# Optimization experiments

Measured on AMD Instinct MI355X. Metric: run time of the kernel, lower is better.

Reference implementation:

```python
import jax, jax.numpy as jnp
import numpy as np

B, N, D = 64, 1024, 512
H, LD = 8, 64            # num_heads, linear_hidden_dim (H*LD == D)
HIDDEN = 4 * D           # ffn_multiply = 4.0
NB = 128                 # number of timestamp buckets
EPS = 1e-6
TS_SCALE = NB / 14.0     # log1p(1e6) ~ 13.8 -> buckets span [0, NB]


def rms_norm(x, eps=EPS):
    return x * jax.lax.rsqrt(jnp.mean(x * x, axis=-1, keepdims=True) + eps)


def setup_inputs() -> dict:
    key = jax.random.key(0)
    ks = jax.random.split(key, 8)
    lengths = np.linspace(256, N, B).astype(np.int64)
    x_offsets = jnp.asarray(np.concatenate([[0], np.cumsum(lengths)]), dtype=jnp.int64)
    T = int(lengths.sum())
    x = jax.random.normal(ks[0], (T, D), dtype=jnp.float32)
    all_timestamps = jnp.sort(jax.random.randint(ks[1], (B, N), 0, 10**6, dtype=jnp.int64), axis=1)
    invalid_attn_mask = jnp.tril(jnp.ones((N, N), jnp.float32))  # causal
    uv = jax.random.normal(ks[2], (D, 3 * H * LD), dtype=jnp.float32) * 0.02
    pos_w = jax.random.normal(ks[3], (2 * N - 1,), dtype=jnp.float32) * 0.02
    ts_w = jax.random.normal(ks[4], (NB + 1,), dtype=jnp.float32) * 0.02
    w_ams = jax.random.normal(ks[5], (2 * H * LD, D), dtype=jnp.float32) * 0.02
    w1 = jax.random.normal(ks[6], (D, HIDDEN), dtype=jnp.float32) * 0.02
    w2 = jax.random.normal(ks[7], (HIDDEN, D), dtype=jnp.float32) * 0.02
    return {"x": x, "x_offsets": x_offsets, "all_timestamps": all_timestamps,
            "invalid_attn_mask": invalid_attn_mask, "uv": uv, "pos_w": pos_w,
            "ts_w": ts_w, "w_ams": w_ams, "w1": w1, "w2": w2}


def reference(x, x_offsets, all_timestamps, invalid_attn_mask, uv, pos_w, ts_w, w_ams, w1, w2):
    T = x.shape[0]
    # RMSNorm (no learned scale, matches F.rms_norm with no weight) + fused proj + SiLU
    proj = jax.nn.silu(rms_norm(x) @ uv)                       # [T, 3*H*LD]
    u, v = proj[:, :2 * H * LD], proj[:, 2 * H * LD:]          # [T,2HD'], [T,HD']
    # jagged -> padded dense
    tok = jnp.arange(T)
    seg = jnp.searchsorted(x_offsets, tok, side="right") - 1   # batch id per token
    pos = tok - x_offsets[seg]                                  # position within sequence
    padded_v = jnp.zeros((B, N, H * LD), v.dtype).at[seg, pos].set(v).reshape(B, N, H, LD)
    # positional relative bias (batch-independent)
    rel = jnp.arange(N)[:, None] - jnp.arange(N)[None, :]
    pos_attn = pos_w[rel + N - 1] * invalid_attn_mask           # [N,N]
    # temporal relative bias: log-bucketized |t_i - t_j|
    dt = jnp.abs(all_timestamps[:, :, None] - all_timestamps[:, None, :]).astype(jnp.float32)
    bucket = jnp.clip(jnp.floor(jnp.log1p(dt) * TS_SCALE), 0, NB).astype(jnp.int32)
    ts_attn = ts_w[bucket] * invalid_attn_mask[None]            # [B,N,N]
    # two-stream bias 'attention' (no softmax)
    out_pos = jnp.einsum("nm,bmhd->bnhd", pos_attn, padded_v)
    out_ts = jnp.einsum("bnm,bmhd->bnhd", ts_attn, padded_v)
    combined = jnp.concatenate([out_pos, out_ts], axis=-1).reshape(B, N, 2 * H * LD)
    attn_out = combined[seg, pos]                               # dense -> jagged, [T, 2*H*LD]
    # gated norm + multistage FFN with residuals
    ams = u * rms_norm(attn_out)
    h = x + ams @ w_ams
    out = h + jax.nn.silu(rms_norm(h) @ w1) @ w2
    return out
```

## Files before the change

kernel.cpp:

```cpp
#include <hip/hip_runtime.h>
#include <cmath>


using u16 = unsigned short;

typedef __bf16 bf16x8 __attribute__((ext_vector_type(8)));
typedef float  f32x4  __attribute__((ext_vector_type(4)));

#define TS_SCALE_F (float)(128.0 / 14.0)

__device__ __forceinline__ u16 f2b(float f) {
  unsigned u = __float_as_uint(f);
  unsigned r = 0x7FFFu + ((u >> 16) & 1u);
  return (u16)((u + r) >> 16);
}
__device__ __forceinline__ float b2f(u16 v) {
  return __uint_as_float(((unsigned)v) << 16);
}
__device__ __forceinline__ bf16x8 as_frag(uint4 r) {
  union { uint4 u; bf16x8 v; } c; c.u = r; return c.v;
}

__device__ __forceinline__ void gload_lds16(const u16* g, u16* l) {
  __builtin_amdgcn_global_load_lds(
      (const __attribute__((address_space(1))) unsigned int*)g,
      (__attribute__((address_space(3))) unsigned int*)l, 16, 0, 0);
}

__device__ __forceinline__ size_t ts_base_elems(int b, int nt) {
  return (size_t)b * 589824 + (size_t)(nt * (nt + 1) / 2) * 16384;
}

__global__ __launch_bounds__(256) void wprep(
    const float* __restrict__ W, u16* __restrict__ Wp, int K, int N)
{
  const int p = blockIdx.x, s = blockIdx.y;
  const int t = threadIdx.x;
  size_t base = ((size_t)p * (K >> 5) + s) * 4096;
  const int e0 = t * 16;
  u16 o[16];
#pragma unroll
  for (int i = 0; i < 16; ++i) {
    int e = e0 + i;
    int kb = e >> 10, r = e & 1023, c = r >> 3, ke = r & 7;
    o[i] = f2b(W[(size_t)(s * 32 + kb * 8 + ke) * N + p * 128 + c]);
  }
  *(uint4*)(Wp + base + e0)     = *(uint4*)o;
  *(uint4*)(Wp + base + e0 + 8) = *(uint4*)(o + 8);
}

#define EPI_SILU_BF16 0
#define EPI_ADD_F32   1

template <int EPI>
__global__ __launch_bounds__(256, 2) void gemm_bf16(
    const u16* __restrict__ A, const u16* __restrict__ Wp,
    void* __restrict__ C, const float* __restrict__ ADD,
    int M, int N, int K)
{
  __shared__ u16 lA[128 * 40];
  __shared__ u16 lB[4096];

  const int tid  = threadIdx.x;
  const int c0b  = blockIdx.x;
  const int t0   = blockIdx.y * 128;
  const int c0   = c0b * 128;
  const int wave = tid >> 6, lane = tid & 63;
  const int wr   = (wave >> 1) * 64, wc = (wave & 1) * 64;
  const int l15  = lane & 15, l4 = lane >> 4;

  f32x4 z = {0.f, 0.f, 0.f, 0.f};
  f32x4 acc[4][4];
#pragma unroll
  for (int m = 0; m < 4; ++m)
#pragma unroll
    for (int j = 0; j < 4; ++j) acc[m][j] = z;

  const int ar = tid >> 1, ak = (tid & 1) * 16;
  const bool arow_ok = (t0 + ar) < M;
  const u16* aptr = A + (size_t)(t0 + ar) * K + ak;
  const int ksteps = K >> 5;
  const u16* wpanel = Wp + (size_t)c0b * ksteps * 4096;
  const u16* wsrc = wpanel + wave * 1024 + lane * 8;
  u16* ldsb = &lB[wave * 1024];

  for (int s = 0; s < ksteps; ++s) {
    uint4 a0 = make_uint4(0, 0, 0, 0), a1 = a0;
    if (arow_ok) {
      a0 = *(const uint4*)(aptr);
      a1 = *(const uint4*)(aptr + 8);
    }
    aptr += 32;
    gload_lds16(wsrc, ldsb);
    gload_lds16(wsrc + 512, ldsb + 512);
    wsrc += 4096;
    *(uint4*)&lA[ar * 40 + ak]     = a0;
    *(uint4*)&lA[ar * 40 + ak + 8] = a1;
    __syncthreads();

    bf16x8 af[4], bfv[4];
#pragma unroll
    for (int m = 0; m < 4; ++m)
      af[m] = as_frag(*(const uint4*)&lA[(wr + m * 16 + l15) * 40 + l4 * 8]);
#pragma unroll
    for (int j = 0; j < 4; ++j)
      bfv[j] = as_frag(*(const uint4*)&lB[(l4 << 10) + (wc + j * 16 + l15) * 8]);
#pragma unroll
    for (int m = 0; m < 4; ++m)
#pragma unroll
      for (int j = 0; j < 4; ++j)
        acc[m][j] = __builtin_amdgcn_mfma_f32_16x16x32_bf16(af[m], bfv[j], acc[m][j], 0, 0, 0);
    __syncthreads();
  }

#pragma unroll
  for (int m = 0; m < 4; ++m) {
#pragma unroll
    for (int r = 0; r < 4; ++r) {
      int row = t0 + wr + m * 16 + l4 * 4 + r;
      if (row >= M) continue;
#pragma unroll
      for (int j = 0; j < 4; ++j) {
        int col = c0 + wc + j * 16 + l15;
        size_t idx = (size_t)row * N + col;
        float y = acc[m][j][r];
        if constexpr (EPI == EPI_SILU_BF16) {
          float s = y / (1.f + __expf(-y));
          ((u16*)C)[idx] = f2b(s);
        } else {
          ((float*)C)[idx] = y + ADD[idx];
        }
      }
    }
  }
}

__global__ __launch_bounds__(128) void pos_scores(
    const float* __restrict__ pos_w, u16* __restrict__ pos_s)
{
  const int n = blockIdx.x;
  const int m0 = threadIdx.x * 8;
  u16 o[8];
#pragma unroll
  for (int i = 0; i < 8; ++i) {
    int m = m0 + i;
    float v = (m <= n) ? pos_w[n - m + 1023] : 0.f;
    o[i] = f2b(v);
  }
  *(uint4*)(pos_s + (size_t)n * 1024 + m0) = *(uint4*)o;
}

__global__ __launch_bounds__(256) void ts_scores(
    const int* __restrict__ tstamp, const float* __restrict__ ts_w,
    u16* __restrict__ ts_s)
{
  const int nt = 7 - (blockIdx.x >> 6);
  const int b  = blockIdx.x & 63;
  const int W  = 128 * (nt + 1);
  const int n0 = nt * 128;
  const int tid = threadIdx.x;

  __shared__ float tsw[132];
  __shared__ int   tsm[1024];
  if (tid < 129) tsw[tid] = ts_w[tid];
  for (int i = tid; i < W; i += 256) tsm[i] = tstamp[b * 1024 + i];
  __syncthreads();

  const int r = tid >> 1, h = tid & 1;
  const int n_abs = n0 + r;
  const int t_n = tstamp[b * 1024 + n_abs];
  u16* row = ts_s + ts_base_elems(b, nt) + (size_t)r * W + h * (W >> 1);
  const int c0 = h * (W >> 1);
  const int half = W >> 1;

  for (int c = 0; c < half; c += 8) {
    u16 o[8];
#pragma unroll
    for (int i = 0; i < 8; ++i) {
      int m = c0 + c + i;
      int d = t_n - tsm[m];
      if (d < 0) d = -d;
      float dt = (float)d;
      int bkt = (int)(log1pf(dt) * TS_SCALE_F);
      bkt = bkt > 128 ? 128 : bkt;
      float v = (m <= n_abs) ? tsw[bkt] : 0.f;
      o[i] = f2b(v);
    }
    *(uint4*)(row + c) = *(uint4*)o;
  }
}

__global__ __launch_bounds__(256, 1) void attn_gemm(
    const u16* __restrict__ proj,
    const int* __restrict__ xoff,
    const u16* __restrict__ pos_s,
    const u16* __restrict__ ts_s,
    u16* __restrict__ attn_out,
    int Ttot)
{
  const int flat = blockIdx.x;
  const int nt = 7 - (flat >> 8);
  const int rem = flat & 255;
  const int b  = rem >> 2;
  const int ct = rem & 3;

  const int off = xoff[b];
  int len = xoff[b + 1] - off;
  if (len < 0) len = 0;
  if (len > 1024) len = 1024;
  if (off < 0 || off + len > Ttot) return;
  const int n0 = nt * 128;
  if (n0 >= len) return;
  const int c0 = ct * 128;
  const int W = 128 * (nt + 1);

  __shared__ u16 lP[128 * 40];
  __shared__ u16 lT[128 * 40];
  __shared__ u16 sV[4096];

  const int tid = threadIdx.x;
  const int wave = tid >> 6, lane = tid & 63;
  const int wr = (wave >> 1) * 64, wc = (wave & 1) * 64;
  const int l15 = lane & 15, l4 = lane >> 4;

  f32x4 z = {0.f, 0.f, 0.f, 0.f};
  f32x4 accP[4][4], accT[4][4];
#pragma unroll
  for (int m = 0; m < 4; ++m)
#pragma unroll
    for (int j = 0; j < 4; ++j) { accP[m][j] = z; accT[m][j] = z; }

  const int ar = tid >> 1, ak = (tid & 1) * 16;
  const u16* pRow = pos_s + (size_t)(n0 + ar) * 1024 + ak;
  const u16* tRow = ts_s + ts_base_elems(b, nt) + (size_t)ar * W + ak;
  const int vk = tid >> 3, vc = (tid & 7) * 16;

  const int mEnd = (n0 + 128 < len) ? (n0 + 128) : len;

  for (int m0 = 0; m0 < mEnd; m0 += 32) {
    {
      int mm = m0 + vk;
      uint4 v0 = make_uint4(0, 0, 0, 0), v1 = v0;
      if (mm < len) {
        const u16* src = proj + (size_t)(off + mm) * 1536 + 1024 + c0 + vc;
        v0 = *(const uint4*)src;
        v1 = *(const uint4*)(src + 8);
      }
      u16 tmp[16];
      *(uint4*)tmp       = v0;
      *(uint4*)(tmp + 8) = v1;
      const int kb = vk >> 3, ke = vk & 7;
#pragma unroll
      for (int i = 0; i < 16; ++i) {
        int col = vc + i;
        int o2 = (kb * 2048 + col * 16 + ke * 2) ^ (((col >> 3) & 7) << 4);
        *(u16*)((char*)sV + o2) = tmp[i];
      }
    }
    {
      uint4 p0 = *(const uint4*)(pRow + m0);
      uint4 p1 = *(const uint4*)(pRow + m0 + 8);
      uint4 t0v = *(const uint4*)(tRow + m0);
      uint4 t1v = *(const uint4*)(tRow + m0 + 8);
      int wb = ar * 40 + ak;
      *(uint4*)&lP[wb]     = p0;
      *(uint4*)&lP[wb + 8] = p1;
      *(uint4*)&lT[wb]     = t0v;
      *(uint4*)&lT[wb + 8] = t1v;
    }
    __syncthreads();

    bf16x8 ap[4], at[4], bv[4];
#pragma unroll
    for (int m = 0; m < 4; ++m) {
      ap[m] = as_frag(*(const uint4*)&lP[(wr + m * 16 + l15) * 40 + l4 * 8]);
      at[m] = as_frag(*(const uint4*)&lT[(wr + m * 16 + l15) * 40 + l4 * 8]);
    }
#pragma unroll
    for (int j = 0; j < 4; ++j) {
      int col = wc + j * 16 + l15;
      int o2 = (l4 * 2048 + col * 16) ^ (((col >> 3) & 7) << 4);
      bv[j] = as_frag(*(const uint4*)((char*)sV + o2));
    }
#pragma unroll
    for (int m = 0; m < 4; ++m)
#pragma unroll
      for (int j = 0; j < 4; ++j) {
        accP[m][j] = __builtin_amdgcn_mfma_f32_16x16x32_bf16(ap[m], bv[j], accP[m][j], 0, 0, 0);
        accT[m][j] = __builtin_amdgcn_mfma_f32_16x16x32_bf16(at[m], bv[j], accT[m][j], 0, 0, 0);
      }
    __syncthreads();
  }

#pragma unroll
  for (int m = 0; m < 4; ++m)
#pragma unroll
    for (int r = 0; r < 4; ++r) {
      int n = n0 + wr + m * 16 + l4 * 4 + r;
      if (n >= len) continue;
      size_t t = (size_t)(off + n);
#pragma unroll
      for (int j = 0; j < 4; ++j) {
        int hd = c0 + wc + j * 16 + l15;
        int colP = ((hd >> 6) << 7) + (hd & 63);
        attn_out[t * 1024 + colP]      = f2b(accP[m][j][r]);
        attn_out[t * 1024 + colP + 64] = f2b(accT[m][j][r]);
      }
    }
}

template <int D, bool HASMUL, bool INBF>
__global__ __launch_bounds__(256) void rms_prep(
    const void* __restrict__ in_, const u16* __restrict__ mul, int mulStride,
    u16* __restrict__ out)
{
  const int row = blockIdx.x;
  const int tid = threadIdx.x;
  const float* rf = (const float*)in_ + (INBF ? 0 : (size_t)row * D);
  const u16*   rb = (const u16*)in_ + (INBF ? (size_t)row * D : 0);
  float ss = 0.f;
#pragma unroll
  for (int i = tid; i < D; i += 256) {
    float v = INBF ? b2f(rb[i]) : rf[i];
    ss += v * v;
  }
#pragma unroll
  for (int o = 32; o > 0; o >>= 1) ss += __shfl_down(ss, o, 64);
  __shared__ float sred[4];
  const int wave = tid >> 6, lane = tid & 63;
  if (lane == 0) sred[wave] = ss;
  __syncthreads();
  float inv = rsqrtf((sred[0] + sred[1] + sred[2] + sred[3]) / (float)D + 1e-6f);
#pragma unroll
  for (int i = tid; i < D; i += 256) {
    float v = (INBF ? b2f(rb[i]) : rf[i]) * inv;
    if constexpr (HASMUL) v *= b2f(mul[(size_t)row * mulStride + i]);
    out[(size_t)row * D + i] = f2b(v);
  }
}

extern "C" void kernel_launch(void* const* d_in, const int* in_sizes, int n_in,
                              void* d_out, int out_size, void* d_ws, size_t ws_size,
                              hipStream_t stream)
{
  const float* x      = (const float*)d_in[0];
  const int*   xoff   = (const int*)d_in[1];
  const int*   tstamp = (const int*)d_in[2];
  const float* uv     = (const float*)d_in[4];
  const float* pos_w  = (const float*)d_in[5];
  const float* ts_w   = (const float*)d_in[6];
  const float* w_ams  = (const float*)d_in[7];
  const float* w1     = (const float*)d_in[8];
  const float* w2     = (const float*)d_in[9];
  const int T = in_sizes[0] / 512;

  char* ws = (char*)d_ws;
  size_t o = 0;
  auto take = [&](size_t bytes) { size_t r = o; o += (bytes + 255) & ~(size_t)255; return r; };

  u16* uvb    = (u16*)(ws + take((size_t)512 * 1536 * 2));
  u16* wamsb  = (u16*)(ws + take((size_t)1024 * 512 * 2));
  u16* w1b    = (u16*)(ws + take((size_t)512 * 2048 * 2));
  u16* w2b    = (u16*)(ws + take((size_t)2048 * 512 * 2));
  u16* posS   = (u16*)(ws + take((size_t)1024 * 1024 * 2));

  size_t tsBytes = (size_t)64 * 589824 * 2;
  size_t s2Bytes = (size_t)T * 1024 * 2;
  if (s2Bytes < tsBytes) s2Bytes = tsBytes;
  size_t o_s2 = take(s2Bytes);
  u16* A1   = (u16*)(ws + o_s2);
  u16* tsS  = (u16*)(ws + o_s2);
  u16* A2   = (u16*)(ws + o_s2);
  u16* mid  = (u16*)(ws + o_s2);

  size_t o_proj = take((size_t)T * 1536 * 2);
  u16* proj = (u16*)(ws + o_proj);
  u16* A1p  = proj + (size_t)T * 1024;

  u16*   attnS = (u16*)d_out;
  float* h     = (float*)d_out;

  if (ws_size < o) return;

  wprep<<<dim3(12, 16), 256, 0, stream>>>(uv,    uvb,   512,  1536);
  wprep<<<dim3(4, 32),  256, 0, stream>>>(w_ams, wamsb, 1024, 512);
  wprep<<<dim3(16, 16), 256, 0, stream>>>(w1,    w1b,   512,  2048);
  wprep<<<dim3(4, 64),  256, 0, stream>>>(w2,    w2b,   2048, 512);

  pos_scores<<<1024, 128, 0, stream>>>(pos_w, posS);

  rms_prep<512, false, false><<<T, 256, 0, stream>>>(x, nullptr, 0, A1);

  dim3 g1(12, (T + 127) / 128);
  gemm_bf16<EPI_SILU_BF16><<<g1, 256, 0, stream>>>(A1, uvb, proj, nullptr, T, 1536, 512);

  ts_scores<<<512, 256, 0, stream>>>(tstamp, ts_w, tsS);

  attn_gemm<<<64 * 32, 256, 0, stream>>>(proj, xoff, posS, tsS, attnS, T);

  rms_prep<1024, true, true><<<T, 256, 0, stream>>>(attnS, proj, 1536, A2);

  dim3 g3(4, (T + 127) / 128);
  gemm_bf16<EPI_ADD_F32><<<g3, 256, 0, stream>>>(A2, wamsb, h, x, T, 512, 1024);

  rms_prep<512, false, false><<<T, 256, 0, stream>>>(h, nullptr, 0, A1p);

  dim3 g4(16, (T + 127) / 128);
  gemm_bf16<EPI_SILU_BF16><<<g4, 256, 0, stream>>>(A1p, w1b, mid, nullptr, T, 2048, 512);

  dim3 g5(4, (T + 127) / 128);
  gemm_bf16<EPI_ADD_F32><<<g5, 256, 0, stream>>>(mid, w2b, h, h, T, 512, 2048);
}
```

Baseline: 939.5 us.

## Fuse RMS-norm scaling into GEMM A-loads, double-buffer GEMM, store ts buckets as u8

```diff
diff --git a/kernel.cpp b/kernel.cpp
--- a/kernel.cpp
+++ b/kernel.cpp
@@ -3,6 +3,7 @@
 
 
 using u16 = unsigned short;
+using u8  = unsigned char;
 
 typedef __bf16 bf16x8 __attribute__((ext_vector_type(8)));
 typedef float  f32x4  __attribute__((ext_vector_type(4)));
@@ -27,7 +28,7 @@
       (__attribute__((address_space(3))) unsigned int*)l, 16, 0, 0);
 }
 
-__device__ __forceinline__ size_t ts_base_elems(int b, int nt) {
+__device__ __forceinline__ size_t ts_base_u8(int b, int nt) {
   return (size_t)b * 589824 + (size_t)(nt * (nt + 1) / 2) * 16384;
 }
 
@@ -51,15 +52,19 @@
 
 #define EPI_SILU_BF16 0
 #define EPI_ADD_F32   1
-
-template <int EPI>
+#define AM_BF16   0
+#define AM_F32S   1
+#define AM_BF16SM 2
+
+template <int EPI, int AMODE>
 __global__ __launch_bounds__(256, 2) void gemm_bf16(
-    const u16* __restrict__ A, const u16* __restrict__ Wp,
-    void* __restrict__ C, const float* __restrict__ ADD,
-    int M, int N, int K)
-{
-  __shared__ u16 lA[128 * 40];
-  __shared__ u16 lB[4096];
+    const u16* __restrict__ A, const float* __restrict__ Af,
+    const float* __restrict__ inv, const u16* __restrict__ U, int ustride,
+    const u16* __restrict__ Wp, void* __restrict__ C,
+    const float* __restrict__ ADD, int M, int N, int K)
+{
+  __shared__ u16 lA[2][128 * 40];
+  __shared__ u16 lB[2][4096];
 
   const int tid  = threadIdx.x;
   const int c0b  = blockIdx.x;
@@ -77,52 +82,100 @@
     for (int j = 0; j < 4; ++j) acc[m][j] = z;
 
   const int ar = tid >> 1, ak = (tid & 1) * 16;
-  const bool arow_ok = (t0 + ar) < M;
-  const u16* aptr = A + (size_t)(t0 + ar) * K + ak;
+  const int row = t0 + ar;
+  const bool arow_ok = row < M;
+  float rinv = 0.f;
+  if (AMODE != AM_BF16 && arow_ok) rinv = inv[row];
+  const u16*   ab = (AMODE != AM_F32S) ? A + (size_t)row * K + ak : nullptr;
+  const float* af = (AMODE == AM_F32S) ? Af + (size_t)row * K + ak : nullptr;
+  const u16*   um = (AMODE == AM_BF16SM) ? U + (size_t)row * ustride + ak : nullptr;
+
+  uint4 pr[4];
+  const uint4 z4 = make_uint4(0, 0, 0, 0);
+
+  auto loadA = [&](int k0) {
+    if (!arow_ok) { pr[0] = z4; pr[1] = z4; pr[2] = z4; pr[3] = z4; return; }
+    if constexpr (AMODE == AM_BF16) {
+      pr[0] = *(const uint4*)(ab + k0);
+      pr[1] = *(const uint4*)(ab + k0 + 8);
+    } else if constexpr (AMODE == AM_F32S) {
+      pr[0] = *(const uint4*)(af + k0);
+      pr[1] = *(const uint4*)(af + k0 + 4);
+      pr[2] = *(const uint4*)(af + k0 + 8);
+      pr[3] = *(const uint4*)(af + k0 + 12);
+    } else {
+      pr[0] = *(const uint4*)(ab + k0);
+      pr[1] = *(const uint4*)(ab + k0 + 8);
+      pr[2] = *(const uint4*)(um + k0);
+      pr[3] = *(const uint4*)(um + k0 + 8);
+    }
+  };
+  auto writeA = [&](u16* dst) {
+    u16 tmp[16];
+    if constexpr (AMODE == AM_BF16) {
+      *(uint4*)tmp       = pr[0];
+      *(uint4*)(tmp + 8) = pr[1];
+    } else if constexpr (AMODE == AM_F32S) {
+      const float* f = (const float*)pr;
+#pragma unroll
+      for (int i = 0; i < 16; ++i) tmp[i] = f2b(f[i] * rinv);
+    } else {
+      const u16* a = (const u16*)pr;
+      const u16* u = (const u16*)(pr + 2);
+#pragma unroll
+      for (int i = 0; i < 16; ++i) tmp[i] = f2b(b2f(a[i]) * rinv * b2f(u[i]));
+    }
+    *(uint4*)(dst + ar * 40 + ak)     = *(uint4*)tmp;
+    *(uint4*)(dst + ar * 40 + ak + 8) = *(uint4*)(tmp + 8);
+  };
+
   const int ksteps = K >> 5;
-  const u16* wpanel = Wp + (size_t)c0b * ksteps * 4096;
-  const u16* wsrc = wpanel + wave * 1024 + lane * 8;
-  u16* ldsb = &lB[wave * 1024];
-
+  const u16* wsrc = Wp + (size_t)c0b * ksteps * 4096 + wave * 1024 + lane * 8;
+
+  loadA(0);
+  gload_lds16(wsrc,       &lB[0][wave * 1024]);
+  gload_lds16(wsrc + 512, &lB[0][wave * 1024 + 512]);
+  wsrc += 4096;
+  writeA(&lA[0][0]);
+  __syncthreads();
+
+  int buf = 0;
   for (int s = 0; s < ksteps; ++s) {
-    uint4 a0 = make_uint4(0, 0, 0, 0), a1 = a0;
-    if (arow_ok) {
-      a0 = *(const uint4*)(aptr);
-      a1 = *(const uint4*)(aptr + 8);
-    }
-    aptr += 32;
-    gload_lds16(wsrc, ldsb);
-    gload_lds16(wsrc + 512, ldsb + 512);
-    wsrc += 4096;
-    *(uint4*)&lA[ar * 40 + ak]     = a0;
-    *(uint4*)&lA[ar * 40 + ak + 8] = a1;
+    if (s + 1 < ksteps) {
+      gload_lds16(wsrc,       &lB[buf ^ 1][wave * 1024]);
+      gload_lds16(wsrc + 512, &lB[buf ^ 1][wave * 1024 + 512]);
+      wsrc += 4096;
+      loadA((s + 1) * 32);
+    }
+    const u16* lAc = &lA[buf][0];
+    const u16* lBc = &lB[buf][0];
+    bf16x8 afr[4], bfv[4];
+#pragma unroll
+    for (int m = 0; m < 4; ++m)
+      afr[m] = as_frag(*(const uint4*)&lAc[(wr + m * 16 + l15) * 40 + l4 * 8]);
+#pragma unroll
+    for (int j = 0; j < 4; ++j)
+      bfv[j] = as_frag(*(const uint4*)&lBc[(l4 << 10) + (wc + j * 16 + l15) * 8]);
+#pragma unroll
+    for (int m = 0; m < 4; ++m)
+#pragma unroll
+      for (int j = 0; j < 4; ++j)
+        acc[m][j] = __builtin_amdgcn_mfma_f32_16x16x32_bf16(afr[m], bfv[j], acc[m][j], 0, 0, 0);
+    if (s + 1 < ksteps) writeA(&lA[buf ^ 1][0]);
     __syncthreads();
-
-    bf16x8 af[4], bfv[4];
-#pragma unroll
-    for (int m = 0; m < 4; ++m)
-      af[m] = as_frag(*(const uint4*)&lA[(wr + m * 16 + l15) * 40 + l4 * 8]);
-#pragma unroll
-    for (int j = 0; j < 4; ++j)
-      bfv[j] = as_frag(*(const uint4*)&lB[(l4 << 10) + (wc + j * 16 + l15) * 8]);
-#pragma unroll
-    for (int m = 0; m < 4; ++m)
-#pragma unroll
-      for (int j = 0; j < 4; ++j)
-        acc[m][j] = __builtin_amdgcn_mfma_f32_16x16x32_bf16(af[m], bfv[j], acc[m][j], 0, 0, 0);
-    __syncthreads();
+    buf ^= 1;
   }
 
 #pragma unroll
   for (int m = 0; m < 4; ++m) {
 #pragma unroll
     for (int r = 0; r < 4; ++r) {
-      int row = t0 + wr + m * 16 + l4 * 4 + r;
-      if (row >= M) continue;
+      int orow = t0 + wr + m * 16 + l4 * 4 + r;
+      if (orow >= M) continue;
 #pragma unroll
       for (int j = 0; j < 4; ++j) {
         int col = c0 + wc + j * 16 + l15;
-        size_t idx = (size_t)row * N + col;
+        size_t idx = (size_t)orow * N + col;
         float y = acc[m][j][r];
         if constexpr (EPI == EPI_SILU_BF16) {
           float s = y / (1.f + __expf(-y));
@@ -150,9 +203,8 @@
   *(uint4*)(pos_s + (size_t)n * 1024 + m0) = *(uint4*)o;
 }
 
-__global__ __launch_bounds__(256) void ts_scores(
-    const int* __restrict__ tstamp, const float* __restrict__ ts_w,
-    u16* __restrict__ ts_s)
+__global__ __launch_bounds__(256) void ts_buckets(
+    const int* __restrict__ tstamp, u8* __restrict__ ts_s)
 {
   const int nt = 7 - (blockIdx.x >> 6);
   const int b  = blockIdx.x & 63;
@@ -160,31 +212,27 @@
   const int n0 = nt * 128;
   const int tid = threadIdx.x;
 
-  __shared__ float tsw[132];
-  __shared__ int   tsm[1024];
-  if (tid < 129) tsw[tid] = ts_w[tid];
+  __shared__ int tsm[1024];
   for (int i = tid; i < W; i += 256) tsm[i] = tstamp[b * 1024 + i];
   __syncthreads();
 
   const int r = tid >> 1, h = tid & 1;
   const int n_abs = n0 + r;
   const int t_n = tstamp[b * 1024 + n_abs];
-  u16* row = ts_s + ts_base_elems(b, nt) + (size_t)r * W + h * (W >> 1);
-  const int c0 = h * (W >> 1);
   const int half = W >> 1;
-
-  for (int c = 0; c < half; c += 8) {
-    u16 o[8];
-#pragma unroll
-    for (int i = 0; i < 8; ++i) {
+  const int c0 = h * half;
+  u8* row = ts_s + ts_base_u8(b, nt) + (size_t)r * W + c0;
+
+  for (int c = 0; c < half; c += 16) {
+    u8 o[16];
+#pragma unroll
+    for (int i = 0; i < 16; ++i) {
       int m = c0 + c + i;
       int d = t_n - tsm[m];
       if (d < 0) d = -d;
-      float dt = (float)d;
-      int bkt = (int)(log1pf(dt) * TS_SCALE_F);
+      int bkt = (int)(log1pf((float)d) * TS_SCALE_F);
       bkt = bkt > 128 ? 128 : bkt;
-      float v = (m <= n_abs) ? tsw[bkt] : 0.f;
-      o[i] = f2b(v);
+      o[i] = (m <= n_abs) ? (u8)bkt : (u8)129;
     }
     *(uint4*)(row + c) = *(uint4*)o;
   }
@@ -194,7 +242,8 @@
     const u16* __restrict__ proj,
     const int* __restrict__ xoff,
     const u16* __restrict__ pos_s,
-    const u16* __restrict__ ts_s,
+    const u8*  __restrict__ tsU8,
+    const float* __restrict__ ts_w,
     u16* __restrict__ attn_out,
     int Ttot)
 {
@@ -217,8 +266,12 @@
   __shared__ u16 lP[128 * 40];
   __shared__ u16 lT[128 * 40];
   __shared__ u16 sV[4096];
+  __shared__ float s_tsw[130];
 
   const int tid = threadIdx.x;
+  if (tid < 130) s_tsw[tid] = (tid < 129) ? ts_w[tid] : 0.f;
+  __syncthreads();
+
   const int wave = tid >> 6, lane = tid & 63;
   const int wr = (wave >> 1) * 64, wc = (wave & 1) * 64;
   const int l15 = lane & 15, l4 = lane >> 4;
@@ -232,7 +285,7 @@
 
   const int ar = tid >> 1, ak = (tid & 1) * 16;
   const u16* pRow = pos_s + (size_t)(n0 + ar) * 1024 + ak;
-  const u16* tRow = ts_s + ts_base_elems(b, nt) + (size_t)ar * W + ak;
+  const u8*  tRow = tsU8 + ts_base_u8(b, nt) + (size_t)ar * W + ak;
   const int vk = tid >> 3, vc = (tid & 7) * 16;
 
   const int mEnd = (n0 + 128 < len) ? (n0 + 128) : len;
@@ -260,13 +313,16 @@
     {
       uint4 p0 = *(const uint4*)(pRow + m0);
       uint4 p1 = *(const uint4*)(pRow + m0 + 8);
-      uint4 t0v = *(const uint4*)(tRow + m0);
-      uint4 t1v = *(const uint4*)(tRow + m0 + 8);
+      uint4 tb = *(const uint4*)(tRow + m0);
+      u16 tt[16];
+      const u8* bp = (const u8*)&tb;
+#pragma unroll
+      for (int i = 0; i < 16; ++i) tt[i] = f2b(s_tsw[bp[i]]);
       int wb = ar * 40 + ak;
       *(uint4*)&lP[wb]     = p0;
       *(uint4*)&lP[wb + 8] = p1;
-      *(uint4*)&lT[wb]     = t0v;
-      *(uint4*)&lT[wb + 8] = t1v;
+      *(uint4*)&lT[wb]     = *(uint4*)tt;
+      *(uint4*)&lT[wb + 8] = *(uint4*)(tt + 8);
     }
     __syncthreads();
 
@@ -309,34 +365,34 @@
     }
 }
 
-template <int D, bool HASMUL, bool INBF>
-__global__ __launch_bounds__(256) void rms_prep(
-    const void* __restrict__ in_, const u16* __restrict__ mul, int mulStride,
-    u16* __restrict__ out)
-{
-  const int row = blockIdx.x;
-  const int tid = threadIdx.x;
-  const float* rf = (const float*)in_ + (INBF ? 0 : (size_t)row * D);
-  const u16*   rb = (const u16*)in_ + (INBF ? (size_t)row * D : 0);
+template <int D, bool F32IN>
+__global__ __launch_bounds__(256) void row_ss(
+    const void* __restrict__ in, float* __restrict__ inv, int T)
+{
+  const int row = blockIdx.x * 4 + (threadIdx.x >> 6);
+  const int lane = threadIdx.x & 63;
+  if (row >= T) return;
   float ss = 0.f;
-#pragma unroll
-  for (int i = tid; i < D; i += 256) {
-    float v = INBF ? b2f(rb[i]) : rf[i];
-    ss += v * v;
+  if constexpr (F32IN) {
+    const float* r = (const float*)in + (size_t)row * D;
+#pragma unroll
+    for (int i = lane * 4; i < D; i += 256) {
+      float4 v = *(const float4*)(r + i);
+      ss += v.x * v.x + v.y * v.y + v.z * v.z + v.w * v.w;
+    }
+  } else {
+    const u16* r = (const u16*)in + (size_t)row * D;
+#pragma unroll
+    for (int i = lane * 8; i < D; i += 512) {
+      uint4 v = *(const uint4*)(r + i);
+      const u16* q = (const u16*)&v;
+#pragma unroll
+      for (int k = 0; k < 8; ++k) { float f = b2f(q[k]); ss += f * f; }
+    }
   }
 #pragma unroll
   for (int o = 32; o > 0; o >>= 1) ss += __shfl_down(ss, o, 64);
-  __shared__ float sred[4];
-  const int wave = tid >> 6, lane = tid & 63;
-  if (lane == 0) sred[wave] = ss;
-  __syncthreads();
-  float inv = rsqrtf((sred[0] + sred[1] + sred[2] + sred[3]) / (float)D + 1e-6f);
-#pragma unroll
-  for (int i = tid; i < D; i += 256) {
-    float v = (INBF ? b2f(rb[i]) : rf[i]) * inv;
-    if constexpr (HASMUL) v *= b2f(mul[(size_t)row * mulStride + i]);
-    out[(size_t)row * D + i] = f2b(v);
-  }
+  if (lane == 0) inv[row] = rsqrtf(ss / (float)D + 1e-6f);
 }
 
 extern "C" void kernel_launch(void* const* d_in, const int* in_sizes, int n_in,
@@ -364,21 +420,18 @@
   u16* w2b    = (u16*)(ws + take((size_t)2048 * 512 * 2));
   u16* posS   = (u16*)(ws + take((size_t)1024 * 1024 * 2));
 
-  size_t tsBytes = (size_t)64 * 589824 * 2;
-  size_t s2Bytes = (size_t)T * 1024 * 2;
-  if (s2Bytes < tsBytes) s2Bytes = tsBytes;
-  size_t o_s2 = take(s2Bytes);
-  u16* A1   = (u16*)(ws + o_s2);
-  u16* tsS  = (u16*)(ws + o_s2);
-  u16* A2   = (u16*)(ws + o_s2);
-  u16* mid  = (u16*)(ws + o_s2);
-
+  size_t o_ts   = take((size_t)64 * 589824);
+  size_t o_attn = take((size_t)T * 1024 * 2);
   size_t o_proj = take((size_t)T * 1536 * 2);
-  u16* proj = (u16*)(ws + o_proj);
-  u16* A1p  = proj + (size_t)T * 1024;
-
-  u16*   attnS = (u16*)d_out;
-  float* h     = (float*)d_out;
+  float* invX = (float*)(ws + take((size_t)T * 4));
+  float* invA = (float*)(ws + take((size_t)T * 4));
+  float* invH = (float*)(ws + take((size_t)T * 4));
+
+  u8*  tsU8  = (u8*)(ws + o_ts);
+  u16* attnS = (u16*)(ws + o_attn);
+  u16* proj  = (u16*)(ws + o_proj);
+  u16* mid   = (u16*)(ws + o_ts);
+  float* h   = (float*)d_out;
 
   if (ws_size < o) return;
 
@@ -388,26 +441,29 @@
   wprep<<<dim3(4, 64),  256, 0, stream>>>(w2,    w2b,   2048, 512);
 
   pos_scores<<<1024, 128, 0, stream>>>(pos_w, posS);
-
-  rms_prep<512, false, false><<<T, 256, 0, stream>>>(x, nullptr, 0, A1);
+  ts_buckets<<<512, 256, 0, stream>>>(tstamp, tsU8);
+
+  row_ss<512, true><<<(T + 3) / 4, 256, 0, stream>>>(x, invX, T);
 
   dim3 g1(12, (T + 127) / 128);
-  gemm_bf16<EPI_SILU_BF16><<<g1, 256, 0, stream>>>(A1, uvb, proj, nullptr, T, 1536, 512);
-
-  ts_scores<<<512, 256, 0, stream>>>(tstamp, ts_w, tsS);
-
-  attn_gemm<<<64 * 32, 256, 0, stream>>>(proj, xoff, posS, tsS, attnS, T);
-
-  rms_prep<1024, true, true><<<T, 256, 0, stream>>>(attnS, proj, 1536, A2);
+  gemm_bf16<EPI_SILU_BF16, AM_F32S><<<g1, 256, 0, stream>>>(
+      nullptr, x, invX, nullptr, 0, uvb, proj, nullptr, T, 1536, 512);
+
+  attn_gemm<<<64 * 32, 256, 0, stream>>>(proj, xoff, posS, tsU8, ts_w, attnS, T);
+
+  row_ss<1024, false><<<(T + 3) / 4, 256, 0, stream>>>(attnS, invA, T);
 
   dim3 g3(4, (T + 127) / 128);
-  gemm_bf16<EPI_ADD_F32><<<g3, 256, 0, stream>>>(A2, wamsb, h, x, T, 512, 1024);
-
-  rms_prep<512, false, false><<<T, 256, 0, stream>>>(h, nullptr, 0, A1p);
+  gemm_bf16<EPI_ADD_F32, AM_BF16SM><<<g3, 256, 0, stream>>>(
+      attnS, nullptr, invA, proj, 1536, wamsb, h, x, T, 512, 1024);
+
+  row_ss<512, true><<<(T + 3) / 4, 256, 0, stream>>>(h, invH, T);
 
   dim3 g4(16, (T + 127) / 128);
-  gemm_bf16<EPI_SILU_BF16><<<g4, 256, 0, stream>>>(A1p, w1b, mid, nullptr, T, 2048, 512);
+  gemm_bf16<EPI_SILU_BF16, AM_F32S><<<g4, 256, 0, stream>>>(
+      nullptr, h, invH, nullptr, 0, w1b, mid, nullptr, T, 2048, 512);
 
   dim3 g5(4, (T + 127) / 128);
-  gemm_bf16<EPI_ADD_F32><<<g5, 256, 0, stream>>>(mid, w2b, h, h, T, 512, 2048);
-}
+  gemm_bf16<EPI_ADD_F32, AM_BF16><<<g5, 256, 0, stream>>>(
+      mid, nullptr, nullptr, nullptr, 0, w2b, h, h, T, 512, 2048);
+}
```

Result: no change. 930.4 us (-1.0%).
